# Performance work log

Hardware: AMD Instinct MI355X
Metric: run time of the kernel (lower is better)

## Reference

```python
import jax, jax.numpy as jnp
import numpy as np

N = 200000      # num nodes
E = 3200000     # num LBO edges (avg degree 16)
FIN = 64
FOUT = 64
K = 6           # Chebyshev order


def setup_inputs() -> dict:
    key = jax.random.key(0)
    k0, k1, k2, k3 = jax.random.split(key, 4)
    x = jax.random.normal(k0, (N, FIN), dtype=jnp.float32)
    LBO_index = jax.random.randint(k1, (2, E), 0, N)
    LBO_weight = jax.random.normal(k2, (E,), dtype=jnp.float32)
    stdv = float(np.sqrt(6.0 / (FIN + FOUT)))  # glorot uniform
    weight = jax.random.uniform(k3, (K, FIN, FOUT), dtype=jnp.float32,
                                minval=-stdv, maxval=stdv)
    bias = jnp.zeros((FOUT,), dtype=jnp.float32)
    return {"x": x, "LBO_index": LBO_index, "LBO_weight": LBO_weight,
            "weight": weight, "bias": bias}


def reference(x, LBO_index, LBO_weight, weight, bias):
    # __norm__: scale Laplacian weights by 2/(-lambda_max), lambda_max = 2.0 (sym)
    lambda_max = jnp.asarray(2.0, dtype=x.dtype)
    w = 2.0 * LBO_weight / (-lambda_max)
    w = jnp.where(w == jnp.inf, 0.0, w)
    # add self loops with fill value -1.0
    loops = jnp.arange(N)
    src = jnp.concatenate([LBO_index[0], loops])   # [E+N]
    dst = jnp.concatenate([LBO_index[1], loops])   # [E+N]
    norm = jnp.concatenate([w, jnp.full((N,), -1.0, dtype=w.dtype)])  # [E+N]

    def prop(z):
        # message = norm * z[src]; aggregate (sum) at dst
        msgs = norm[:, None] * z[src]                      # [E+N, F]
        return jax.ops.segment_sum(msgs, dst, num_segments=N)

    # Chebyshev recursion: T0 = x, T1 = L_hat x, Tk = 2 L_hat T_{k-1} - T_{k-2}
    Tx0 = x
    out = jnp.matmul(x, weight[0])
    Tx1 = prop(x)
    out = out + jnp.matmul(Tx1, weight[1])
    for k in range(2, K):
        Tx2 = 2.0 * prop(Tx1) - Tx0
        out = out + jnp.matmul(Tx2, weight[k])
        Tx0, Tx1 = Tx1, Tx2
    return out + bias
```

## Files before the change

kernel.cpp:

```cpp
#include <hip/hip_runtime.h>
#include <hip/hip_fp16.h>

#define FDIM 64
#define NB_SHIFT 10
#define NB_PAD 256
#define CH 4096

typedef __attribute__((ext_vector_type(8))) _Float16 half8;
typedef __attribute__((ext_vector_type(4))) float floatx4;


__global__ void hist_kernel(const int* __restrict__ dst, int* __restrict__ counts, int E) {
    int e = blockIdx.x * blockDim.x + threadIdx.x;
    if (e < E) atomicAdd(&counts[dst[e]], 1);
}

__global__ void scan_block_kernel(const int* __restrict__ in, int* __restrict__ out,
                                  int* __restrict__ blockSums, int n) {
    __shared__ int sdata[256];
    int t = threadIdx.x;
    int base = blockIdx.x * 1024 + t * 4;
    int v0 = (base + 0 < n) ? in[base + 0] : 0;
    int v1 = (base + 1 < n) ? in[base + 1] : 0;
    int v2 = (base + 2 < n) ? in[base + 2] : 0;
    int v3 = (base + 3 < n) ? in[base + 3] : 0;
    int tsum = v0 + v1 + v2 + v3;
    sdata[t] = tsum;
    __syncthreads();
    for (int off = 1; off < 256; off <<= 1) {
        int x = (t >= off) ? sdata[t - off] : 0;
        __syncthreads();
        sdata[t] += x;
        __syncthreads();
    }
    if (t == 255) blockSums[blockIdx.x] = sdata[255];
    int run = sdata[t] - tsum;
    if (base + 0 < n) out[base + 0] = run; run += v0;
    if (base + 1 < n) out[base + 1] = run; run += v1;
    if (base + 2 < n) out[base + 2] = run; run += v2;
    if (base + 3 < n) out[base + 3] = run;
}

__global__ void add_off_kernel(int* __restrict__ row_start, const int* __restrict__ blockSums,
                               int* __restrict__ bucket_cursor, int n) {
    int i = blockIdx.x * blockDim.x + threadIdx.x;
    if (i < n) {
        int v = row_start[i] + blockSums[i >> 10];
        row_start[i] = v;
        if ((i & ((1 << NB_SHIFT) - 1)) == 0) bucket_cursor[i >> NB_SHIFT] = v;
    }
}

__global__ __launch_bounds__(256) void bin_kernel(
        const int* __restrict__ src, const int* __restrict__ dst,
        const float* __restrict__ w, int* __restrict__ bucket_cursor,
        int2* __restrict__ binned_sv, unsigned short* __restrict__ binned_d,
        int E, int NB) {
    __shared__ int2 stage_sv[CH];
    __shared__ int  stage_d[CH];
    __shared__ int hist[NB_PAD], offs0[NB_PAD], run[NB_PAD], base[NB_PAD];

    int t = threadIdx.x;
    int c0 = blockIdx.x * CH;
    int valid = E - c0; if (valid > CH) valid = CH;

    for (int b = t; b < NB_PAD; b += 256) hist[b] = 0;
    __syncthreads();

    int  myd[16];
    int2 mysv[16];
    #pragma unroll
    for (int j = 0; j < 16; ++j) {
        int i = t + j * 256;
        if (i < valid) {
            int e = c0 + i;
            int d = dst[e];
            myd[j] = d;
            mysv[j] = make_int2(src[e], __float_as_int(-w[e]));
            atomicAdd(&hist[d >> NB_SHIFT], 1);
        } else myd[j] = -1;
    }
    __syncthreads();

    offs0[t] = hist[t];
    __syncthreads();
    for (int off = 1; off < 256; off <<= 1) {
        int x = (t >= off) ? offs0[t - off] : 0;
        __syncthreads();
        offs0[t] += x;
        __syncthreads();
    }
    int cnt_b = hist[t];
    int excl = offs0[t] - cnt_b;
    __syncthreads();
    offs0[t] = excl;
    run[t] = excl;
    base[t] = (t < NB && cnt_b > 0) ? atomicAdd(&bucket_cursor[t], cnt_b) : 0;
    __syncthreads();

    #pragma unroll
    for (int j = 0; j < 16; ++j) {
        if (myd[j] >= 0) {
            int b = myd[j] >> NB_SHIFT;
            int pos = atomicAdd(&run[b], 1);
            stage_sv[pos] = mysv[j];
            stage_d[pos]  = myd[j];
        }
    }
    __syncthreads();

    for (int i = t; i < valid; i += 256) {
        int d = stage_d[i];
        int b = d >> NB_SHIFT;
        int g = base[b] + (i - offs0[b]);
        binned_sv[g] = stage_sv[i];
        binned_d[g]  = (unsigned short)(d & ((1 << NB_SHIFT) - 1));
    }
}

__global__ __launch_bounds__(1024) void csr_kernel(
        const int* __restrict__ row_start, const int2* __restrict__ binned_sv,
        const unsigned short* __restrict__ binned_d,
        int2* __restrict__ colval, int E, int N) {
    __shared__ int lcur[1 << NB_SHIFT];
    int b = blockIdx.x;
    int t = threadIdx.x;
    int nbase = b << NB_SHIFT;
    int nextNode = (b + 1) << NB_SHIFT;

    int nloc = N - nbase; if (nloc > (1 << NB_SHIFT)) nloc = 1 << NB_SHIFT;
    if (t < nloc) lcur[t] = row_start[nbase + t];
    __syncthreads();

    int lo = row_start[nbase];
    int hi = (nextNode < N) ? row_start[nextNode] : E;
    for (int i = lo + t; i < hi; i += 1024) {
        int2 sv = binned_sv[i];
        int ld = binned_d[i];
        int p = atomicAdd(&lcur[ld], 1);
        colval[p] = sv;
    }
}


__global__ void convert_kernel(const float* __restrict__ x, __half* __restrict__ XH,
                               int total) {
    int i = (blockIdx.x * blockDim.x + threadIdx.x) * 4;
    if (i < total) {
        float4 v = *(const float4*)(x + i);
        __half2 h0 = __floats2half2_rn(v.x, v.y);
        __half2 h1 = __floats2half2_rn(v.z, v.w);
        int2 packed = make_int2(*(int*)&h0, *(int*)&h1);
        *(int2*)((char*)XH + (size_t)i * 2) = packed;
    }
}


__global__ void prep_wt_kernel(const float* __restrict__ W, __half* __restrict__ WT,
                               int K) {
    int i = blockIdx.x * blockDim.x + threadIdx.x;
    if (i < K * FDIM * FDIM) {
        int tk  = i / (FDIM * FDIM);
        int rem = i - tk * FDIM * FDIM;
        int fin = rem >> 6;
        int o   = rem & 63;
        float sig = (float)(1 << (2 * tk));
        WT[(size_t)o * (K * FDIM) + tk * FDIM + fin] = __float2half(sig * W[i]);
    }
}


#define GATHER_LOOP(SRC, ACC)                                                       \
    {                                                                               \
        int m = (cnt < 64) ? cnt : 64;                                              \
        int2 my = (lane < m) ? cv[lane] : make_int2(0, 0);                          \
        int cx = my.x;                                                              \
        float vv = __int_as_float(my.y);                                            \
        int j = 0;                                                                  \
        for (; j + 8 <= m; j += 8) {                                                \
            int c0 = __shfl(cx, j+0); float v0 = __shfl(vv, j+0);                   \
            int c1 = __shfl(cx, j+1); float v1 = __shfl(vv, j+1);                   \
            int c2 = __shfl(cx, j+2); float v2 = __shfl(vv, j+2);                   \
            int c3 = __shfl(cx, j+3); float v3 = __shfl(vv, j+3);                   \
            int c4 = __shfl(cx, j+4); float v4 = __shfl(vv, j+4);                   \
            int c5 = __shfl(cx, j+5); float v5 = __shfl(vv, j+5);                   \
            int c6 = __shfl(cx, j+6); float v6 = __shfl(vv, j+6);                   \
            int c7 = __shfl(cx, j+7); float v7 = __shfl(vv, j+7);                   \
            float t0 = __half2float(SRC[(size_t)c0 * FDIM + lane]);                 \
            float t1 = __half2float(SRC[(size_t)c1 * FDIM + lane]);                 \
            float t2 = __half2float(SRC[(size_t)c2 * FDIM + lane]);                 \
            float t3 = __half2float(SRC[(size_t)c3 * FDIM + lane]);                 \
            float t4 = __half2float(SRC[(size_t)c4 * FDIM + lane]);                 \
            float t5 = __half2float(SRC[(size_t)c5 * FDIM + lane]);                 \
            float t6 = __half2float(SRC[(size_t)c6 * FDIM + lane]);                 \
            float t7 = __half2float(SRC[(size_t)c7 * FDIM + lane]);                 \
            ACC += v0*t0 + v1*t1 + v2*t2 + v3*t3 + v4*t4 + v5*t5 + v6*t6 + v7*t7;   \
        }                                                                           \
        for (; j < m; ++j) {                                                        \
            int c = __shfl(cx, j); float v = __shfl(vv, j);                         \
            ACC += v * __half2float(SRC[(size_t)c * FDIM + lane]);                  \
        }                                                                           \
        for (int e2 = 64; e2 < cnt; ++e2) {                \
            int2 a = cv[e2];                                                        \
            ACC += __int_as_float(a.y) * __half2float(SRC[(size_t)a.x * FDIM + lane]); \
        }                                                                           \
    }

__global__ __launch_bounds__(256, 8) void pass1_kernel(
        const __half* __restrict__ XH, const int* __restrict__ row_start,
        const int* __restrict__ counts, const int2* __restrict__ colval,
        __half* __restrict__ T1H, int N) {
    int wid = threadIdx.x >> 6;
    int lane = threadIdx.x & 63;
    int node = blockIdx.x * 4 + wid;
    if (node >= N) return;

    float acc = -__half2float(XH[(size_t)node * FDIM + lane]);
    int s = row_start[node];
    int cnt = counts[node];
    const int2* cv = colval + s;
    GATHER_LOOP(XH, acc)
    T1H[(size_t)node * FDIM + lane] = __float2half(acc * 0.25f);
}

__global__ __launch_bounds__(256, 8) void passk_kernel(
        const __half* __restrict__ TcH, const __half* __restrict__ TpH,
        __half* __restrict__ TnH, const int* __restrict__ row_start,
        const int* __restrict__ counts, const int2* __restrict__ colval, int N) {
    int wid = threadIdx.x >> 6;
    int lane = threadIdx.x & 63;
    int node = blockIdx.x * 4 + wid;
    if (node >= N) return;

    size_t self = (size_t)node * FDIM + lane;
    int s = row_start[node];
    int cnt = counts[node];
    const int2* cv = colval + s;
    float acc = -__half2float(TcH[self]);
    GATHER_LOOP(TcH, acc)
    float tns = 0.5f * acc - 0.0625f * __half2float(TpH[self]);
    TnH[self] = __float2half(tns);
}


__global__ __launch_bounds__(256) void final_mfma_kernel(
        const __half* __restrict__ Tall, const __half* __restrict__ WT,
        const float* __restrict__ bias, float* __restrict__ out,
        int N, int K) {
    int wid = threadIdx.x >> 6;
    int lane = threadIdx.x & 63;
    int tile = blockIdx.x * 4 + wid;
    int nodeBase = tile << 4;
    if (nodeBase >= N) return;
    size_t NT = (size_t)N * FDIM;
    int Kflat = K * FDIM;

    int m = lane & 15;
    int kgrp = lane >> 4;
    int nodeA = nodeBase + m;
    bool aok = nodeA < N;

    floatx4 acc[4];
    #pragma unroll
    for (int f = 0; f < 4; ++f) {
        float bv = bias[f * 16 + m];
        acc[f] = (floatx4){bv, bv, bv, bv};
    }

    for (int kc = 0; kc < Kflat / 32; ++kc) {
        int tk = kc >> 1;
        int feat = ((kc & 1) << 5) + (kgrp << 3);
        half8 a = aok ? *(const half8*)(Tall + (size_t)tk * NT + (size_t)nodeA * FDIM + feat)
                      : (half8)(_Float16)0;
        int kOff = (kc << 5) + (kgrp << 3);
        #pragma unroll
        for (int f = 0; f < 4; ++f) {
            half8 b = *(const half8*)(WT + (size_t)(f * 16 + m) * Kflat + kOff);
            acc[f] = __builtin_amdgcn_mfma_f32_16x16x32_f16(a, b, acc[f], 0, 0, 0);
        }
    }

    #pragma unroll
    for (int f = 0; f < 4; ++f) {
        #pragma unroll
        for (int r = 0; r < 4; ++r) {
            int nrow = nodeBase + (kgrp << 2) + r;
            if (nrow < N) out[(size_t)nrow * FDIM + f * 16 + m] = acc[f][r];
        }
    }
}


extern "C" void kernel_launch(void* const* d_in, const int* in_sizes, int n_in,
                              void* d_out, int out_size, void* d_ws, size_t ws_size,
                              hipStream_t stream) {
    const float* x      = (const float*)d_in[0];
    const int*   idx    = (const int*)d_in[1];
    const float* w      = (const float*)d_in[2];
    const float* weight = (const float*)d_in[3];
    const float* bias   = (const float*)d_in[4];
    float* out = (float*)d_out;

    const int N = in_sizes[0] / FDIM;
    const int E = in_sizes[2];
    const int K = in_sizes[3] / (FDIM * FDIM);
    const int NB = (N + (1 << NB_SHIFT) - 1) >> NB_SHIFT;

    const int* src = idx;
    const int* dst = idx + E;

    int* counts        = (int*)d_ws;
    int* row_start     = counts + N;
    int* blockSums     = row_start + N;
    int* bucket_cursor = blockSums + 512;
    int2* colval       = (int2*)(bucket_cursor + 256);
    __half* Tall       = (__half*)(colval + E);
    __half* WT         = Tall + (size_t)K * N * FDIM;
    int2* binned_sv    = (int2*)Tall;
    unsigned short* binned_d = (unsigned short*)(Tall + (size_t)N * FDIM);

    hipMemsetAsync(counts, 0, (size_t)N * sizeof(int), stream);

    int eb = (E + 255) / 256;
    hist_kernel<<<eb, 256, 0, stream>>>(dst, counts, E);

    int nb = (N + 1023) / 1024;
    scan_block_kernel<<<nb, 256, 0, stream>>>(counts, row_start, blockSums, N);
    scan_block_kernel<<<1, 256, 0, stream>>>(blockSums, blockSums, blockSums + 500, nb);
    add_off_kernel<<<(N + 255) / 256, 256, 0, stream>>>(row_start, blockSums,
                                                        bucket_cursor, N);

    int bb = (E + CH - 1) / CH;
    bin_kernel<<<bb, 256, 0, stream>>>(src, dst, w, bucket_cursor,
                                       binned_sv, binned_d, E, NB);
    csr_kernel<<<NB, 1024, 0, stream>>>(row_start, binned_sv, binned_d,
                                        colval, E, N);

    convert_kernel<<<(N * FDIM + 1023) / 1024, 256, 0, stream>>>(x, Tall, N * FDIM);
    prep_wt_kernel<<<(K * FDIM * FDIM + 255) / 256, 256, 0, stream>>>(weight, WT, K);

    size_t NT = (size_t)N * FDIM;
    __half* T[8];
    for (int k = 0; k < K && k < 8; ++k) T[k] = Tall + (size_t)k * NT;

    int pb = (N + 3) / 4;
    pass1_kernel<<<pb, 256, 0, stream>>>(T[0], row_start, counts, colval, T[1], N);
    for (int k = 2; k < K; ++k) {
        passk_kernel<<<pb, 256, 0, stream>>>(T[k-1], T[k-2], T[k], row_start, counts,
                                             colval, N);
    }

    int tiles = (N + 15) >> 4;
    final_mfma_kernel<<<(tiles + 3) / 4, 256, 0, stream>>>(Tall, WT, bias, out, N, K);
}
```

Baseline: 841.6 us.

## Build CSR row offsets per bucket instead of a global per-node histogram and scan

Replaces the per-edge global atomic histogram over N nodes and the three-kernel global scan with a coarse 256-bucket histogram in shared memory plus a single-block bucket scan. Per-node counts and row starts are now computed inside the CSR kernel, using a shared-memory histogram and a 1024-wide scan over each bucket's binned edges. This removes 3.2M global atomics, the N-sized memset and several launches. In exchange the CSR kernel makes an extra pass over binned_d and runs a longer in-block scan.

```diff
diff --git a/kernel.cpp b/kernel.cpp
--- a/kernel.cpp
+++ b/kernel.cpp
@@ -10,45 +10,37 @@
 typedef __attribute__((ext_vector_type(4))) float floatx4;
 
 
-__global__ void hist_kernel(const int* __restrict__ dst, int* __restrict__ counts, int E) {
-    int e = blockIdx.x * blockDim.x + threadIdx.x;
-    if (e < E) atomicAdd(&counts[dst[e]], 1);
-}
-
-__global__ void scan_block_kernel(const int* __restrict__ in, int* __restrict__ out,
-                                  int* __restrict__ blockSums, int n) {
-    __shared__ int sdata[256];
+__global__ __launch_bounds__(256) void bucket_hist_kernel(
+        const int* __restrict__ dst, int* __restrict__ bucket_cnt, int E) {
+    __shared__ int h[NB_PAD];
+    for (int i = threadIdx.x; i < NB_PAD; i += 256) h[i] = 0;
+    __syncthreads();
+    int stride = gridDim.x * 256;
+    for (int e = blockIdx.x * 256 + threadIdx.x; e < E; e += stride)
+        atomicAdd(&h[dst[e] >> NB_SHIFT], 1);
+    __syncthreads();
+    for (int i = threadIdx.x; i < NB_PAD; i += 256)
+        if (h[i]) atomicAdd(&bucket_cnt[i], h[i]);
+}
+
+__global__ __launch_bounds__(256) void bucket_scan_kernel(
+        const int* __restrict__ bucket_cnt, int* __restrict__ bucket_base,
+        int* __restrict__ bucket_cursor) {
+    __shared__ int s[NB_PAD];
     int t = threadIdx.x;
-    int base = blockIdx.x * 1024 + t * 4;
-    int v0 = (base + 0 < n) ? in[base + 0] : 0;
-    int v1 = (base + 1 < n) ? in[base + 1] : 0;
-    int v2 = (base + 2 < n) ? in[base + 2] : 0;
-    int v3 = (base + 3 < n) ? in[base + 3] : 0;
-    int tsum = v0 + v1 + v2 + v3;
-    sdata[t] = tsum;
+    int v = bucket_cnt[t];
+    s[t] = v;
     __syncthreads();
     for (int off = 1; off < 256; off <<= 1) {
-        int x = (t >= off) ? sdata[t - off] : 0;
-        __syncthreads();
-        sdata[t] += x;
-        __syncthreads();
-    }
-    if (t == 255) blockSums[blockIdx.x] = sdata[255];
-    int run = sdata[t] - tsum;
-    if (base + 0 < n) out[base + 0] = run; run += v0;
-    if (base + 1 < n) out[base + 1] = run; run += v1;
-    if (base + 2 < n) out[base + 2] = run; run += v2;
-    if (base + 3 < n) out[base + 3] = run;
-}
-
-__global__ void add_off_kernel(int* __restrict__ row_start, const int* __restrict__ blockSums,
-                               int* __restrict__ bucket_cursor, int n) {
-    int i = blockIdx.x * blockDim.x + threadIdx.x;
-    if (i < n) {
-        int v = row_start[i] + blockSums[i >> 10];
-        row_start[i] = v;
-        if ((i & ((1 << NB_SHIFT) - 1)) == 0) bucket_cursor[i >> NB_SHIFT] = v;
-    }
+        int x = (t >= off) ? s[t - off] : 0;
+        __syncthreads();
+        s[t] += x;
+        __syncthreads();
+    }
+    int excl = s[t] - v;
+    bucket_base[t] = excl;
+    if (t == 255) bucket_base[256] = s[255];
+    bucket_cursor[t] = excl;
 }
 
 __global__ __launch_bounds__(256) void bin_kernel(
@@ -119,25 +111,46 @@
 }
 
 __global__ __launch_bounds__(1024) void csr_kernel(
-        const int* __restrict__ row_start, const int2* __restrict__ binned_sv,
+        const int* __restrict__ bucket_base, const int2* __restrict__ binned_sv,
         const unsigned short* __restrict__ binned_d,
-        int2* __restrict__ colval, int E, int N) {
-    __shared__ int lcur[1 << NB_SHIFT];
+        int* __restrict__ row_start, int* __restrict__ counts,
+        int2* __restrict__ colval, int N) {
+    __shared__ int lhist[1 << NB_SHIFT];
+    __shared__ int lscan[1 << NB_SHIFT];
     int b = blockIdx.x;
     int t = threadIdx.x;
     int nbase = b << NB_SHIFT;
-    int nextNode = (b + 1) << NB_SHIFT;
-
-    int nloc = N - nbase; if (nloc > (1 << NB_SHIFT)) nloc = 1 << NB_SHIFT;
-    if (t < nloc) lcur[t] = row_start[nbase + t];
-    __syncthreads();
-
-    int lo = row_start[nbase];
-    int hi = (nextNode < N) ? row_start[nextNode] : E;
+    int lo = bucket_base[b];
+    int hi = bucket_base[b + 1];
+
+    lhist[t] = 0;
+    __syncthreads();
+    for (int i = lo + t; i < hi; i += 1024)
+        atomicAdd(&lhist[binned_d[i]], 1);
+    __syncthreads();
+
+    int v = lhist[t];
+    lscan[t] = v;
+    __syncthreads();
+    for (int off = 1; off < 1024; off <<= 1) {
+        int x = (t >= off) ? lscan[t - off] : 0;
+        __syncthreads();
+        lscan[t] += x;
+        __syncthreads();
+    }
+    int rs = lo + lscan[t] - v;
+    int node = nbase + t;
+    if (node < N) {
+        row_start[node] = rs;
+        counts[node] = v;
+    }
+    __syncthreads();
+    lscan[t] = rs;
+    __syncthreads();
+
     for (int i = lo + t; i < hi; i += 1024) {
         int2 sv = binned_sv[i];
-        int ld = binned_d[i];
-        int p = atomicAdd(&lcur[ld], 1);
+        int p = atomicAdd(&lscan[binned_d[i]], 1);
         colval[p] = sv;
     }
 }
@@ -311,30 +324,25 @@
 
     int* counts        = (int*)d_ws;
     int* row_start     = counts + N;
-    int* blockSums     = row_start + N;
-    int* bucket_cursor = blockSums + 512;
-    int2* colval       = (int2*)(bucket_cursor + 256);
+    int* bucket_cnt    = row_start + N;
+    int* bucket_base   = bucket_cnt + 256;
+    int* bucket_cursor = bucket_base + 260;
+    int2* colval       = (int2*)(bucket_cursor + 256 + 4);
     __half* Tall       = (__half*)(colval + E);
     __half* WT         = Tall + (size_t)K * N * FDIM;
     int2* binned_sv    = (int2*)Tall;
     unsigned short* binned_d = (unsigned short*)(Tall + (size_t)N * FDIM);
 
-    hipMemsetAsync(counts, 0, (size_t)N * sizeof(int), stream);
-
-    int eb = (E + 255) / 256;
-    hist_kernel<<<eb, 256, 0, stream>>>(dst, counts, E);
-
-    int nb = (N + 1023) / 1024;
-    scan_block_kernel<<<nb, 256, 0, stream>>>(counts, row_start, blockSums, N);
-    scan_block_kernel<<<1, 256, 0, stream>>>(blockSums, blockSums, blockSums + 500, nb);
-    add_off_kernel<<<(N + 255) / 256, 256, 0, stream>>>(row_start, blockSums,
-                                                        bucket_cursor, N);
+    hipMemsetAsync(bucket_cnt, 0, 256 * sizeof(int), stream);
+
+    bucket_hist_kernel<<<512, 256, 0, stream>>>(dst, bucket_cnt, E);
+    bucket_scan_kernel<<<1, 256, 0, stream>>>(bucket_cnt, bucket_base, bucket_cursor);
 
     int bb = (E + CH - 1) / CH;
     bin_kernel<<<bb, 256, 0, stream>>>(src, dst, w, bucket_cursor,
                                        binned_sv, binned_d, E, NB);
-    csr_kernel<<<NB, 1024, 0, stream>>>(row_start, binned_sv, binned_d,
-                                        colval, E, N);
+    csr_kernel<<<NB, 1024, 0, stream>>>(bucket_base, binned_sv, binned_d,
+                                        row_start, counts, colval, N);
 
     convert_kernel<<<(N * FDIM + 1023) / 1024, 256, 0, stream>>>(x, Tall, N * FDIM);
     prep_wt_kernel<<<(K * FDIM * FDIM + 255) / 256, 256, 0, stream>>>(weight, WT, K);
```

Measured after the change: 820.8 us. 2.5% less time.
